# Performance work log

Measured on AMD Instinct MI355X. Metric: run time of the kernel, lower is better.

## Reference

```python
import jax, jax.numpy as jnp
import numpy as np

B_, N, C, H = 2048, 49, 384, 12
WH, WW = 7, 7
HEAD_DIM = C // H
SCALE = HEAD_DIM ** -0.5
TABLE = (2 * WH - 1) * (2 * WW - 1)  # 169


def _relative_position_index():
    coords = np.stack(np.meshgrid(np.arange(WH), np.arange(WW), indexing='ij'))  # [2,Wh,Ww]
    flat = coords.reshape(2, -1)  # [2,N]
    rel = flat[:, :, None] - flat[:, None, :]  # [2,N,N]
    rel = rel.transpose(1, 2, 0).astype(np.int32)  # [N,N,2]
    rel[:, :, 0] += WH - 1
    rel[:, :, 1] += WW - 1
    rel[:, :, 0] *= 2 * WW - 1
    return rel.sum(-1)  # [N,N] int32 in [0,169)


def setup_inputs() -> dict:
    key = jax.random.key(0)
    ks = jax.random.split(key, 8)
    return {
        'x': jax.random.normal(ks[0], (B_, N, C), jnp.float32),
        'mask': jax.random.normal(ks[1], (B_, 1, N, N), jnp.float32),
        'stagein': jax.random.uniform(ks[2], (B_, N, C), jnp.float32),
        'rel_bias_table': jax.random.normal(ks[3], (TABLE, H), jnp.float32) * 0.02,
        'rel_pos_index': jnp.asarray(_relative_position_index()),
        'qkv_w': jax.random.normal(ks[4], (3 * C, C), jnp.float32) * 0.02,
        'qkv_b': jax.random.normal(ks[5], (3 * C,), jnp.float32) * 0.02,
        'proj_w': jax.random.normal(ks[6], (C, C), jnp.float32) * 0.02,
        'proj_b': jax.random.normal(ks[7], (C,), jnp.float32) * 0.02,
    }


def reference(x, mask, stagein, rel_bias_table, rel_pos_index, qkv_w, qkv_b, proj_w, proj_b):
    x = x * stagein  # stagein is not None branch
    qkv = x @ qkv_w.T + qkv_b  # [B_, N, 3C]
    qkv = qkv.reshape(B_, N, 3, H, HEAD_DIM).transpose(2, 0, 3, 1, 4)  # [3,B_,H,N,hd]
    q, k, v = qkv[0], qkv[1], qkv[2]
    q = q * SCALE
    attn = jnp.einsum('bhnd,bhmd->bhnm', q, k)  # [B_,H,N,N]
    # relative position bias gather: [N*N] -> [N,N,H] -> [1,H,N,N]
    bias = rel_bias_table[rel_pos_index.reshape(-1)].reshape(N, N, H)
    bias = bias.transpose(2, 0, 1)[None]
    attn = jax.nn.softmax(attn + bias + mask, axis=-1)
    out = jnp.einsum('bhnm,bhmd->bhnd', attn, v)  # [B_,H,N,hd]
    out = out.transpose(0, 2, 1, 3).reshape(B_, N, C)
    return out @ proj_w.T + proj_b
```

## Files before the change

### kernel.cpp

```cpp
#include <hip/hip_runtime.h>
#include <hip/hip_bf16.h>
#include <stdint.h>

#define NWIN 2048
#define NTOK 49
#define CDIM 384
#define NHEAD 12
#define HD 32
#define C3 1152
#define NN2 2401
#define MROWS 100352

typedef __bf16 bf16x8 __attribute__((ext_vector_type(8)));
typedef float f32x4 __attribute__((ext_vector_type(4)));
typedef uint32_t u32x4 __attribute__((ext_vector_type(4)));

static __device__ __forceinline__ unsigned short f2bf(float f) {
  uint32_t u = __builtin_bit_cast(uint32_t, f);
  u += 0x7fffu + ((u >> 16) & 1u);
  return (unsigned short)(u >> 16);
}

static __device__ __forceinline__ void gload_lds16(const void* g, void* l) {
  __builtin_amdgcn_global_load_lds((const __attribute__((address_space(1))) void*)g,
                                   (__attribute__((address_space(3))) void*)l,
                                   16, 0, 0);
}

static __device__ __forceinline__ bf16x8 zero8() {
  u32x4 z = {0u, 0u, 0u, 0u};
  return __builtin_bit_cast(bf16x8, z);
}

__global__ void prep_kernel(const float* __restrict__ qkv_w, const float* __restrict__ proj_w,
                            const float* __restrict__ table, const int* __restrict__ idx,
                            unsigned short* __restrict__ wq, unsigned short* __restrict__ wp,
                            float* __restrict__ biasexp) {
  const int NW1 = C3 * CDIM;
  const int NW2 = CDIM * CDIM;
  const int NB = NHEAD * NN2;
  int i = blockIdx.x * blockDim.x + threadIdx.x;
  int stride = gridDim.x * blockDim.x;
  for (int t = i; t < NW1 + NW2 + NB; t += stride) {
    if (t < NW1) {
      wq[t] = f2bf(qkv_w[t]);
    } else if (t < NW1 + NW2) {
      int j = t - NW1;
      wp[j] = f2bf(proj_w[j]);
    } else {
      int j = t - NW1 - NW2;
      int h = j / NN2;
      int nm = j - h * NN2;
      biasexp[j] = table[idx[nm] * NHEAD + h];
    }
  }
}

__global__ void mul_kernel(const float4* __restrict__ x, const float4* __restrict__ s,
                           u32x4* __restrict__ A, int n8) {
  int i0 = blockIdx.x * blockDim.x + threadIdx.x;
  int stride = gridDim.x * blockDim.x;
  for (int t = i0; t < n8; t += stride) {
    float4 a0 = x[2 * t], a1 = x[2 * t + 1];
    float4 b0 = s[2 * t], b1 = s[2 * t + 1];
    union { unsigned short us[8]; u32x4 v; } o;
    o.us[0] = f2bf(a0.x * b0.x); o.us[1] = f2bf(a0.y * b0.y);
    o.us[2] = f2bf(a0.z * b0.z); o.us[3] = f2bf(a0.w * b0.w);
    o.us[4] = f2bf(a1.x * b1.x); o.us[5] = f2bf(a1.y * b1.y);
    o.us[6] = f2bf(a1.z * b1.z); o.us[7] = f2bf(a1.w * b1.w);
    A[t] = o.v;
  }
}

__launch_bounds__(256, 2)
__global__ void qkv_gemm(const unsigned short* __restrict__ A,
                         const unsigned short* __restrict__ Bw,
                         const float* __restrict__ qkvb,
                         unsigned short* __restrict__ qo,
                         unsigned short* __restrict__ ko,
                         unsigned short* __restrict__ vo) {
  __shared__ unsigned short As[128 * 64];
  __shared__ unsigned short Bs[128 * 64];
  const int tid = threadIdx.x;
  const int w = tid >> 6, l = tid & 63;
  const int l15 = l & 15, lhi = l >> 4;
  const int wgid = (blockIdx.x & 7) * 882 + (blockIdx.x >> 3);
  const int mt = wgid / 9, nt = wgid - mt * 9;
  const int wr = w >> 1, wc = w & 1;
  const int srow = tid >> 3;
  const int scb = (tid & 7) ^ (srow & 7);
  const unsigned short* Ag = A + (size_t)(mt * 128 + srow) * CDIM + scb * 8;
  const unsigned short* Bg = Bw + (size_t)(nt * 128 + srow) * CDIM + scb * 8;
  unsigned short* Asl = As + srow * 64 + (tid & 7) * 8;
  unsigned short* Bsl = Bs + srow * 64 + (tid & 7) * 8;
  const f32x4 z4 = {0.f, 0.f, 0.f, 0.f};
  f32x4 acc[4][4];
#pragma unroll
  for (int m = 0; m < 4; ++m)
#pragma unroll
    for (int n = 0; n < 4; ++n) acc[m][n] = z4;
  const int xr = l15 & 7;
  for (int kt = 0; kt < 6; ++kt) {
    const unsigned short* ag = Ag + kt * 64;
    const unsigned short* bg = Bg + kt * 64;
#pragma unroll
    for (int i = 0; i < 4; ++i) {
      gload_lds16(ag + i * 32 * CDIM, Asl + i * 2048);
      gload_lds16(bg + i * 32 * CDIM, Bsl + i * 2048);
    }
    __syncthreads();
#pragma unroll
    for (int kk = 0; kk < 2; ++kk) {
      const int sl = ((kk << 2) | lhi) ^ xr;
      bf16x8 af[4], bfr[4];
#pragma unroll
      for (int m = 0; m < 4; ++m)
        af[m] = *(const bf16x8*)(As + (wr * 64 + m * 16 + l15) * 64 + sl * 8);
#pragma unroll
      for (int n = 0; n < 4; ++n)
        bfr[n] = *(const bf16x8*)(Bs + (wc * 64 + n * 16 + l15) * 64 + sl * 8);
#pragma unroll
      for (int m = 0; m < 4; ++m)
#pragma unroll
        for (int n = 0; n < 4; ++n)
          acc[m][n] = __builtin_amdgcn_mfma_f32_16x16x32_bf16(af[m], bfr[n], acc[m][n], 0, 0, 0);
    }
    __syncthreads();
  }
  const float SCALE_F = 0.17677669529663687f;
  const int six = nt * 2 + wc;
  const int which = six / 6;
  const int cbase = (six - which * 6) * 64;
  unsigned short* outw = (which == 0) ? qo : ((which == 1) ? ko : vo);
  const float* bptr = qkvb + which * CDIM;
#pragma unroll
  for (int m = 0; m < 4; ++m) {
#pragma unroll
    for (int j = 0; j < 4; ++j) {
      const int r = mt * 128 + wr * 64 + m * 16 + lhi * 4 + j;
      const int bwin = r / 49;
      const int ntok = r - bwin * 49;
#pragma unroll
      for (int n = 0; n < 4; ++n) {
        const int c = cbase + n * 16 + l15;
        const int h = c >> 5, d = c & 31;
        float val = acc[m][n][j] + bptr[c];
        if (which == 0) val *= SCALE_F;
        outw[(((size_t)bwin * NHEAD + h) * NTOK + ntok) * HD + d] = f2bf(val);
      }
    }
  }
}

__launch_bounds__(256, 2)
__global__ void attn_kernel(const unsigned short* __restrict__ q,
                            const unsigned short* __restrict__ kmat,
                            const unsigned short* __restrict__ vmat,
                            const float* __restrict__ mask,
                            const float* __restrict__ biasexp,
                            unsigned short* __restrict__ attnout) {
  __shared__ unsigned short P_lds[4][64 * 72];
  __shared__ unsigned short vT_lds[4][32 * 72];
  const int tid = threadIdx.x;
  const int w = tid >> 6, l = tid & 63;
  const int l15 = l & 15, lhi = l >> 4;
  const int b = blockIdx.x;
  unsigned short* Pw = &P_lds[w][0];
  unsigned short* Vw = &vT_lds[w][0];
  const float* maskb = mask + (size_t)b * NN2;
  const f32x4 z4 = {0.f, 0.f, 0.f, 0.f};
  for (int it = 0; it < 3; ++it) {
    const int h = it * 4 + w;
    const size_t hb = ((size_t)b * NHEAD + h) * NTOK * HD;
    const unsigned short* qb = q + hb;
    const unsigned short* kb = kmat + hb;
    const unsigned short* vb = vmat + hb;
    {
      const int n = l;
      unsigned short tmp[32];
      if (n < 49) {
        *(u32x4*)(&tmp[0])  = *(const u32x4*)(vb + n * 32);
        *(u32x4*)(&tmp[8])  = *(const u32x4*)(vb + n * 32 + 8);
        *(u32x4*)(&tmp[16]) = *(const u32x4*)(vb + n * 32 + 16);
        *(u32x4*)(&tmp[24]) = *(const u32x4*)(vb + n * 32 + 24);
      } else {
#pragma unroll
        for (int d2 = 0; d2 < 32; ++d2) tmp[d2] = 0;
      }
#pragma unroll
      for (int d2 = 0; d2 < 32; ++d2) Vw[d2 * 72 + n] = tmp[d2];
    }
    bf16x8 aq[4], bk[4];
#pragma unroll
    for (int t = 0; t < 4; ++t) {
      const int row = t * 16 + l15;
      if (row < 49) {
        aq[t] = *(const bf16x8*)(qb + row * 32 + lhi * 8);
        bk[t] = *(const bf16x8*)(kb + row * 32 + lhi * 8);
      } else {
        aq[t] = zero8();
        bk[t] = zero8();
      }
    }
    f32x4 s[4][4];
#pragma unroll
    for (int ti = 0; ti < 4; ++ti)
#pragma unroll
      for (int tj = 0; tj < 4; ++tj)
        s[ti][tj] = __builtin_amdgcn_mfma_f32_16x16x32_bf16(aq[ti], bk[tj], z4, 0, 0, 0);
    const float* biash = biasexp + h * NN2;
#pragma unroll
    for (int ti = 0; ti < 4; ++ti) {
#pragma unroll
      for (int r = 0; r < 4; ++r) {
        const int n = ti * 16 + lhi * 4 + r;
#pragma unroll
        for (int tj = 0; tj < 4; ++tj) {
          const int m = tj * 16 + l15;
          float val = -1e30f;
          if (n < 49 && m < 49)
            val = s[ti][tj][r] + biash[n * 49 + m] + maskb[n * 49 + m];
          s[ti][tj][r] = val;
        }
      }
    }
#pragma unroll
    for (int ti = 0; ti < 4; ++ti) {
#pragma unroll
      for (int r = 0; r < 4; ++r) {
        float mx = fmaxf(fmaxf(s[ti][0][r], s[ti][1][r]), fmaxf(s[ti][2][r], s[ti][3][r]));
        mx = fmaxf(mx, __shfl_xor(mx, 1));
        mx = fmaxf(mx, __shfl_xor(mx, 2));
        mx = fmaxf(mx, __shfl_xor(mx, 4));
        mx = fmaxf(mx, __shfl_xor(mx, 8));
        float e0 = __expf(s[ti][0][r] - mx);
        float e1 = __expf(s[ti][1][r] - mx);
        float e2 = __expf(s[ti][2][r] - mx);
        float e3 = __expf(s[ti][3][r] - mx);
        float sum = (e0 + e1) + (e2 + e3);
        sum += __shfl_xor(sum, 1);
        sum += __shfl_xor(sum, 2);
        sum += __shfl_xor(sum, 4);
        sum += __shfl_xor(sum, 8);
        const float rinv = 1.0f / sum;
        const int n = ti * 16 + lhi * 4 + r;
        unsigned short* pr = Pw + n * 72 + l15;
        pr[0]  = f2bf(e0 * rinv);
        pr[16] = f2bf(e1 * rinv);
        pr[32] = f2bf(e2 * rinv);
        pr[48] = f2bf(e3 * rinv);
      }
    }
    f32x4 o[4][2];
#pragma unroll
    for (int ti = 0; ti < 4; ++ti) { o[ti][0] = z4; o[ti][1] = z4; }
#pragma unroll
    for (int kk = 0; kk < 2; ++kk) {
      bf16x8 pa[4], bv[2];
#pragma unroll
      for (int ti = 0; ti < 4; ++ti)
        pa[ti] = *(const bf16x8*)(Pw + (ti * 16 + l15) * 72 + kk * 32 + lhi * 8);
#pragma unroll
      for (int dj = 0; dj < 2; ++dj)
        bv[dj] = *(const bf16x8*)(Vw + (dj * 16 + l15) * 72 + kk * 32 + lhi * 8);
#pragma unroll
      for (int ti = 0; ti < 4; ++ti)
#pragma unroll
        for (int dj = 0; dj < 2; ++dj)
          o[ti][dj] = __builtin_amdgcn_mfma_f32_16x16x32_bf16(pa[ti], bv[dj], o[ti][dj], 0, 0, 0);
    }
#pragma unroll
    for (int ti = 0; ti < 4; ++ti) {
#pragma unroll
      for (int r = 0; r < 4; ++r) {
        const int n = ti * 16 + lhi * 4 + r;
        if (n < 49) {
          unsigned short* orow = attnout + ((size_t)b * NTOK + n) * CDIM + h * HD;
          orow[l15] = f2bf(o[ti][0][r]);
          orow[16 + l15] = f2bf(o[ti][1][r]);
        }
      }
    }
  }
}

__launch_bounds__(256, 2)
__global__ void proj_gemm(const unsigned short* __restrict__ A,
                          const unsigned short* __restrict__ Bw,
                          const float* __restrict__ pb,
                          float* __restrict__ out) {
  __shared__ unsigned short As[128 * 64];
  __shared__ unsigned short Bs[128 * 64];
  const int tid = threadIdx.x;
  const int w = tid >> 6, l = tid & 63;
  const int l15 = l & 15, lhi = l >> 4;
  const int wgid = (blockIdx.x & 7) * 294 + (blockIdx.x >> 3);
  const int mt = wgid / 3, nt = wgid - mt * 3;
  const int wr = w >> 1, wc = w & 1;
  const int srow = tid >> 3;
  const int scb = (tid & 7) ^ (srow & 7);
  const unsigned short* Ag = A + (size_t)(mt * 128 + srow) * CDIM + scb * 8;
  const unsigned short* Bg = Bw + (size_t)(nt * 128 + srow) * CDIM + scb * 8;
  unsigned short* Asl = As + srow * 64 + (tid & 7) * 8;
  unsigned short* Bsl = Bs + srow * 64 + (tid & 7) * 8;
  const f32x4 z4 = {0.f, 0.f, 0.f, 0.f};
  f32x4 acc[4][4];
#pragma unroll
  for (int m = 0; m < 4; ++m)
#pragma unroll
    for (int n = 0; n < 4; ++n) acc[m][n] = z4;
  const int xr = l15 & 7;
  for (int kt = 0; kt < 6; ++kt) {
    const unsigned short* ag = Ag + kt * 64;
    const unsigned short* bg = Bg + kt * 64;
#pragma unroll
    for (int i = 0; i < 4; ++i) {
      gload_lds16(ag + i * 32 * CDIM, Asl + i * 2048);
      gload_lds16(bg + i * 32 * CDIM, Bsl + i * 2048);
    }
    __syncthreads();
#pragma unroll
    for (int kk = 0; kk < 2; ++kk) {
      const int sl = ((kk << 2) | lhi) ^ xr;
      bf16x8 af[4], bfr[4];
#pragma unroll
      for (int m = 0; m < 4; ++m)
        af[m] = *(const bf16x8*)(As + (wr * 64 + m * 16 + l15) * 64 + sl * 8);
#pragma unroll
      for (int n = 0; n < 4; ++n)
        bfr[n] = *(const bf16x8*)(Bs + (wc * 64 + n * 16 + l15) * 64 + sl * 8);
#pragma unroll
      for (int m = 0; m < 4; ++m)
#pragma unroll
        for (int n = 0; n < 4; ++n)
          acc[m][n] = __builtin_amdgcn_mfma_f32_16x16x32_bf16(af[m], bfr[n], acc[m][n], 0, 0, 0);
    }
    __syncthreads();
  }
#pragma unroll
  for (int m = 0; m < 4; ++m) {
#pragma unroll
    for (int j = 0; j < 4; ++j) {
      const int r = mt * 128 + wr * 64 + m * 16 + lhi * 4 + j;
      float* orow = out + (size_t)r * CDIM;
#pragma unroll
      for (int n = 0; n < 4; ++n) {
        const int c = nt * 128 + wc * 64 + n * 16 + l15;
        orow[c] = acc[m][n][j] + pb[c];
      }
    }
  }
}

extern "C" void kernel_launch(void* const* d_in, const int* in_sizes, int n_in,
                              void* d_out, int out_size, void* d_ws, size_t ws_size,
                              hipStream_t stream) {
  const float* x       = (const float*)d_in[0];
  const float* mask    = (const float*)d_in[1];
  const float* stagein = (const float*)d_in[2];
  const float* table   = (const float*)d_in[3];
  const int*   idx     = (const int*)d_in[4];
  const float* qkv_w   = (const float*)d_in[5];
  const float* qkv_b   = (const float*)d_in[6];
  const float* proj_w  = (const float*)d_in[7];
  const float* proj_b  = (const float*)d_in[8];
  float* out = (float*)d_out;
  char* ws = (char*)d_ws;

  const size_t SZA = (size_t)MROWS * CDIM * 2;
  unsigned short* Abf = (unsigned short*)(ws);
  unsigned short* qb  = (unsigned short*)(ws + SZA);
  unsigned short* kb  = (unsigned short*)(ws + 2 * SZA);
  unsigned short* vb  = (unsigned short*)(ws + 3 * SZA);
  unsigned short* wq  = (unsigned short*)(ws + 4 * SZA);
  unsigned short* wp  = (unsigned short*)(ws + 4 * SZA + (size_t)C3 * CDIM * 2);
  float* biasexp      = (float*)(ws + 4 * SZA + (size_t)C3 * CDIM * 2 + (size_t)CDIM * CDIM * 2);
  unsigned short* attnout = Abf;

  prep_kernel<<<dim3(512), dim3(256), 0, stream>>>(qkv_w, proj_w, table, idx, wq, wp, biasexp);
  mul_kernel<<<dim3(2048), dim3(256), 0, stream>>>((const float4*)x, (const float4*)stagein,
                                                   (u32x4*)Abf, MROWS * CDIM / 8);
  qkv_gemm<<<dim3(784 * 9), dim3(256), 0, stream>>>(Abf, wq, qkv_b, qb, kb, vb);
  attn_kernel<<<dim3(NWIN), dim3(256), 0, stream>>>(qb, kb, vb, mask, biasexp, attnout);
  proj_gemm<<<dim3(784 * 3), dim3(256), 0, stream>>>(attnout, wp, proj_b, out);
}
```

Before: 452.1 us.

## Fuse stagein multiply and bf16 conversion into QKV GEMM A-tile load

```diff
diff --git a/kernel.cpp b/kernel.cpp
--- a/kernel.cpp
+++ b/kernel.cpp
@@ -19,6 +19,10 @@
   uint32_t u = __builtin_bit_cast(uint32_t, f);
   u += 0x7fffu + ((u >> 16) & 1u);
   return (unsigned short)(u >> 16);
+}
+
+static __device__ __forceinline__ uint32_t pk2(float a, float b) {
+  return (uint32_t)f2bf(a) | ((uint32_t)f2bf(b) << 16);
 }
 
 static __device__ __forceinline__ void gload_lds16(const void* g, void* l) {
@@ -56,24 +60,9 @@
   }
 }
 
-__global__ void mul_kernel(const float4* __restrict__ x, const float4* __restrict__ s,
-                           u32x4* __restrict__ A, int n8) {
-  int i0 = blockIdx.x * blockDim.x + threadIdx.x;
-  int stride = gridDim.x * blockDim.x;
-  for (int t = i0; t < n8; t += stride) {
-    float4 a0 = x[2 * t], a1 = x[2 * t + 1];
-    float4 b0 = s[2 * t], b1 = s[2 * t + 1];
-    union { unsigned short us[8]; u32x4 v; } o;
-    o.us[0] = f2bf(a0.x * b0.x); o.us[1] = f2bf(a0.y * b0.y);
-    o.us[2] = f2bf(a0.z * b0.z); o.us[3] = f2bf(a0.w * b0.w);
-    o.us[4] = f2bf(a1.x * b1.x); o.us[5] = f2bf(a1.y * b1.y);
-    o.us[6] = f2bf(a1.z * b1.z); o.us[7] = f2bf(a1.w * b1.w);
-    A[t] = o.v;
-  }
-}
-
 __launch_bounds__(256, 2)
-__global__ void qkv_gemm(const unsigned short* __restrict__ A,
+__global__ void qkv_gemm(const float* __restrict__ x,
+                         const float* __restrict__ stg,
                          const unsigned short* __restrict__ Bw,
                          const float* __restrict__ qkvb,
                          unsigned short* __restrict__ qo,
@@ -87,11 +76,15 @@
   const int wgid = (blockIdx.x & 7) * 882 + (blockIdx.x >> 3);
   const int mt = wgid / 9, nt = wgid - mt * 9;
   const int wr = w >> 1, wc = w & 1;
+  const int arow = tid >> 1;
+  const int ahalf = tid & 1;
+  const float* xg = x   + (size_t)(mt * 128 + arow) * CDIM + ahalf * 32;
+  const float* sg = stg + (size_t)(mt * 128 + arow) * CDIM + ahalf * 32;
+  unsigned short* Asw = As + arow * 64;
+  const int arow7 = arow & 7;
   const int srow = tid >> 3;
   const int scb = (tid & 7) ^ (srow & 7);
-  const unsigned short* Ag = A + (size_t)(mt * 128 + srow) * CDIM + scb * 8;
   const unsigned short* Bg = Bw + (size_t)(nt * 128 + srow) * CDIM + scb * 8;
-  unsigned short* Asl = As + srow * 64 + (tid & 7) * 8;
   unsigned short* Bsl = Bs + srow * 64 + (tid & 7) * 8;
   const f32x4 z4 = {0.f, 0.f, 0.f, 0.f};
   f32x4 acc[4][4];
@@ -101,12 +94,26 @@
     for (int n = 0; n < 4; ++n) acc[m][n] = z4;
   const int xr = l15 & 7;
   for (int kt = 0; kt < 6; ++kt) {
-    const unsigned short* ag = Ag + kt * 64;
     const unsigned short* bg = Bg + kt * 64;
 #pragma unroll
-    for (int i = 0; i < 4; ++i) {
-      gload_lds16(ag + i * 32 * CDIM, Asl + i * 2048);
+    for (int i = 0; i < 4; ++i)
       gload_lds16(bg + i * 32 * CDIM, Bsl + i * 2048);
+    {
+      const float4* xp = (const float4*)(xg + kt * 64);
+      const float4* sp = (const float4*)(sg + kt * 64);
+      float4 xv[8], sv[8];
+#pragma unroll
+      for (int i = 0; i < 8; ++i) { xv[i] = xp[i]; sv[i] = sp[i]; }
+#pragma unroll
+      for (int g = 0; g < 4; ++g) {
+        u32x4 o;
+        o[0] = pk2(xv[2 * g].x * sv[2 * g].x,     xv[2 * g].y * sv[2 * g].y);
+        o[1] = pk2(xv[2 * g].z * sv[2 * g].z,     xv[2 * g].w * sv[2 * g].w);
+        o[2] = pk2(xv[2 * g + 1].x * sv[2 * g + 1].x, xv[2 * g + 1].y * sv[2 * g + 1].y);
+        o[3] = pk2(xv[2 * g + 1].z * sv[2 * g + 1].z, xv[2 * g + 1].w * sv[2 * g + 1].w);
+        const int ps = (ahalf * 4 + g) ^ arow7;
+        *(u32x4*)(Asw + ps * 8) = o;
+      }
     }
     __syncthreads();
 #pragma unroll
@@ -368,19 +375,16 @@
   char* ws = (char*)d_ws;
 
   const size_t SZA = (size_t)MROWS * CDIM * 2;
-  unsigned short* Abf = (unsigned short*)(ws);
+  unsigned short* attnout = (unsigned short*)(ws);
   unsigned short* qb  = (unsigned short*)(ws + SZA);
   unsigned short* kb  = (unsigned short*)(ws + 2 * SZA);
   unsigned short* vb  = (unsigned short*)(ws + 3 * SZA);
   unsigned short* wq  = (unsigned short*)(ws + 4 * SZA);
   unsigned short* wp  = (unsigned short*)(ws + 4 * SZA + (size_t)C3 * CDIM * 2);
   float* biasexp      = (float*)(ws + 4 * SZA + (size_t)C3 * CDIM * 2 + (size_t)CDIM * CDIM * 2);
-  unsigned short* attnout = Abf;
 
   prep_kernel<<<dim3(512), dim3(256), 0, stream>>>(qkv_w, proj_w, table, idx, wq, wp, biasexp);
-  mul_kernel<<<dim3(2048), dim3(256), 0, stream>>>((const float4*)x, (const float4*)stagein,
-                                                   (u32x4*)Abf, MROWS * CDIM / 8);
-  qkv_gemm<<<dim3(784 * 9), dim3(256), 0, stream>>>(Abf, wq, qkv_b, qb, kb, vb);
+  qkv_gemm<<<dim3(784 * 9), dim3(256), 0, stream>>>(x, stagein, wq, qkv_b, qb, kb, vb);
   attn_kernel<<<dim3(NWIN), dim3(256), 0, stream>>>(qb, kb, vb, mask, biasexp, attnout);
   proj_gemm<<<dim3(784 * 3), dim3(256), 0, stream>>>(attnout, wp, proj_b, out);
 }
```

New measurement: 978.5 us. +116.5%, slower.
